# Optimization experiments

Hardware: AMD Instinct MI355X
Metric: run time of the kernel (lower is better)

## Reference

```python
import jax, jax.numpy as jnp
import numpy as np


def setup_inputs() -> dict:
    key = jax.random.key(0)
    B, T, FFT, HOP = 16, 2048, 1024, 256
    n_bins = FFT // 2 + 1  # 513
    stfts = jax.random.normal(key, (B, T, n_bins, 2), dtype=jnp.float32)
    return {"stfts": stfts, "frame_length": FFT, "frame_step": HOP, "fft_length": FFT}


def reference(stfts, frame_length, frame_step, fft_length):
    # --- precomputed constants (built in the layer's build()) ---
    n = jnp.arange(fft_length, dtype=jnp.float32)
    angles = (2.0 * np.pi / fft_length) * (n[:, None] * n[None, :])  # [fft, fft]
    idft_cos = jnp.cos(angles)
    idft_sin = jnp.sin(angles)
    # periodic Hann window
    t = jnp.arange(frame_length, dtype=jnp.float32)
    window = 0.5 - 0.5 * jnp.cos(2.0 * np.pi * t / frame_length)
    hop_ratio = frame_step / frame_length
    normalization = np.sqrt(1.0 / (1.0 - hop_ratio + 1e-8))
    syn_window = window / np.float32(normalization)
    if fft_length > frame_length:
        syn_window = jnp.pad(syn_window, (0, fft_length - frame_length))

    # --- forward ---
    real_part = stfts[..., 0]  # [B, T, n_bins]
    imag_part = stfts[..., 1]
    if fft_length % 2 == 0:
        mirror_real = real_part[:, :, 1:-1]
        mirror_imag = imag_part[:, :, 1:-1]
    else:
        mirror_real = real_part[:, :, 1:]
        mirror_imag = imag_part[:, :, 1:]
    full_real = jnp.concatenate([real_part, mirror_real[:, :, ::-1]], axis=-1)   # [B, T, fft]
    full_imag = jnp.concatenate([imag_part, -mirror_imag[:, :, ::-1]], axis=-1)  # [B, T, fft]

    # explicit IDFT via dense matmul (transpose_b in TF; matrices are symmetric)
    time_real = jnp.einsum('btf,nf->btn', full_real, idft_cos)
    time_real = time_real - jnp.einsum('btf,nf->btn', full_imag, idft_sin)
    time_real = time_real / jnp.float32(fft_length)

    windowed = (time_real * syn_window[None, None, :])[:, :, :frame_length]  # [B, T, frame_length]

    # overlap-and-add
    B, T, L = windowed.shape
    out_len = (T - 1) * frame_step + frame_length
    idx = jnp.arange(T)[:, None] * frame_step + jnp.arange(L)[None, :]  # [T, L]
    out = jnp.zeros((B, out_len), dtype=windowed.dtype).at[:, idx].add(windowed)
    return out
```

## Files before the change

kernel.cpp:

```cpp
#include <hip/hip_runtime.h>
#include <math.h>


#define BATCH  16
#define TFR    2048
#define NB     513
#define HOP    256
#define OUTLEN 525056
#define TROWS  2051
#define OWN    32
#define NBLK   65
#define OLALEN (OWN * HOP)
#define OLAPAD (OLALEN + OLALEN / 16)

#define NTHR   512
#define NWAVE  8

#define PIDX(n) ((n) + ((n) >> 4))

#define TWO_PI 6.2831853071795864f
#define WSCALE 8.456302966727588e-4f

__device__ __forceinline__ float2 cadd(float2 a, float2 b){ return make_float2(a.x+b.x, a.y+b.y); }
__device__ __forceinline__ float2 csub(float2 a, float2 b){ return make_float2(a.x-b.x, a.y-b.y); }
__device__ __forceinline__ float2 cmul(float2 a, float2 b){ return make_float2(a.x*b.x - a.y*b.y, a.x*b.y + a.y*b.x); }

__global__ __launch_bounds__(NTHR)
void istft_rfft(const float2* __restrict__ stfts, float* __restrict__ out)
{
    __shared__ float ola[OLAPAD];

    const int tid  = threadIdx.x;
    const int lane = tid & 63;
    const int wave = tid >> 6;

    const int b  = blockIdx.x / NBLK;
    const int ib = blockIdx.x - b * NBLK;
    const int T0 = ib * OWN;

    for (int i = tid; i < OLAPAD; i += NTHR) ola[i] = 0.f;

    float2 ptw[8];
    #pragma unroll
    for (int r = 0; r < 8; ++r) {
        float s, c;
        sincosf(TWO_PI * (float)(lane + 64 * r) * (1.0f / 1024.0f), &s, &c);
        ptw[r] = make_float2(c, s);
    }
    float2 om[8];
    om[0] = make_float2(1.f, 0.f);
    { float s, c; sincosf(TWO_PI * (float)lane * (1.0f / 512.0f), &s, &c); om[1] = make_float2(c, s); }
    #pragma unroll
    for (int m = 2; m < 8; ++m) om[m] = cmul(om[m - 1], om[1]);
    float2 twc[5];
    #pragma unroll
    for (int s = 0; s < 5; ++s) {
        const int h = 32 >> s;
        float sn, cs;
        sincosf(TWO_PI * (float)(lane & (h - 1)) / (float)(2 * h), &sn, &cs);
        twc[s] = (lane & h) ? make_float2(cs, sn) : make_float2(1.f, 0.f);
    }
    const int brl = ((lane & 1) << 5) | ((lane & 2) << 3) | ((lane & 4) << 1)
                  | ((lane & 8) >> 1) | ((lane & 16) >> 3) | ((lane & 32) >> 5);
    const int n0 = brl * 16;
    float win[16];
    #pragma unroll
    for (int j = 0; j < 16; ++j)
        win[j] = (0.5f - 0.5f * cosf(TWO_PI * (float)(n0 + j) * (1.0f / 1024.0f))) * WSCALE;

    __syncthreads();

    const int tmin = (T0 - 3 > 0) ? T0 - 3 : 0;
    const int tmax = (T0 + OWN - 1 < TFR - 1) ? T0 + OWN - 1 : TFR - 1;
    const int srcl = (64 - lane) & 63;

    for (int t = tmin + wave; t <= tmax; t += NWAVE) {
        const float2* Xg = stfts + (size_t)(b * TFR + t) * NB;

        float2 X[8];
        #pragma unroll
        for (int r = 0; r < 8; ++r) X[r] = Xg[lane + 64 * r];
        const float2 X512 = Xg[512];

        float2 Z[8];
        #pragma unroll
        for (int r = 0; r < 8; ++r) {
            float2 mv;
            mv.x = __shfl(X[7 - r].x, srcl);
            mv.y = __shfl(X[7 - r].y, srcl);
            const float2 fix = (r == 0) ? X512 : X[(8 - r) & 7];
            if (lane == 0) mv = fix;
            float Yy = X[r].y, Cy = -mv.y;
            if (lane == 0 && r == 0) { Yy = 0.f; Cy = 0.f; }
            const float Sx = X[r].x + mv.x, Sy = Yy + Cy;
            const float Dx = X[r].x - mv.x, Dy = Yy - Cy;
            const float2 W = ptw[r];
            const float ex = W.x * Dx - W.y * Dy;
            const float ey = W.x * Dy + W.y * Dx;
            Z[r] = make_float2(Sx - ey, Sy + ex);
        }

        float2 u[8];
        {
            const float2 t0 = cadd(Z[0], Z[4]), t1 = csub(Z[0], Z[4]);
            const float2 t2 = cadd(Z[2], Z[6]), t3 = csub(Z[2], Z[6]);
            const float2 t4 = cadd(Z[1], Z[5]), t5 = csub(Z[1], Z[5]);
            const float2 t6 = cadd(Z[3], Z[7]), t7 = csub(Z[3], Z[7]);
            const float2 E0 = cadd(t0, t2), E2 = csub(t0, t2);
            const float2 E1 = make_float2(t1.x - t3.y, t1.y + t3.x);
            const float2 E3 = make_float2(t1.x + t3.y, t1.y - t3.x);
            const float2 O0 = cadd(t4, t6), O2 = csub(t4, t6);
            const float2 O1 = make_float2(t5.x - t7.y, t5.y + t7.x);
            const float2 O3 = make_float2(t5.x + t7.y, t5.y - t7.x);
            const float cc = 0.70710678118654752f;
            const float2 W1O1 = make_float2(cc * (O1.x - O1.y), cc * (O1.x + O1.y));
            const float2 iO2  = make_float2(-O2.y, O2.x);
            const float2 W3O3 = make_float2(cc * (-O3.x - O3.y), cc * (O3.x - O3.y));
            u[0] = cadd(E0, O0);   u[4] = csub(E0, O0);
            u[1] = cadd(E1, W1O1); u[5] = csub(E1, W1O1);
            u[2] = cadd(E2, iO2);  u[6] = csub(E2, iO2);
            u[3] = cadd(E3, W3O3); u[7] = csub(E3, W3O3);
        }
        #pragma unroll
        for (int m = 1; m < 8; ++m) u[m] = cmul(u[m], om[m]);

        #pragma unroll
        for (int s = 0; s < 6; ++s) {
            const int h = 32 >> s;
            const bool lo = (lane & h) == 0;
            #pragma unroll
            for (int m = 0; m < 8; ++m) {
                const float sx = __shfl_xor(u[m].x, h);
                const float sy = __shfl_xor(u[m].y, h);
                float2 w;
                w.x = sx + (lo ? u[m].x : -u[m].x);
                w.y = sy + (lo ? u[m].y : -u[m].y);
                u[m] = (h > 1) ? cmul(w, twc[s]) : w;
            }
        }

        const int base = (t - T0) * HOP + n0;
        if ((unsigned)base < OLALEN) {
            const int pb = PIDX(base);
            #pragma unroll
            for (int m = 0; m < 8; ++m) {
                atomicAdd(&ola[pb + 2 * m],     u[m].x * win[2 * m]);
                atomicAdd(&ola[pb + 2 * m + 1], u[m].y * win[2 * m + 1]);
            }
        }
    }

    __syncthreads();

    const int ownRows = (TROWS - T0 < OWN) ? (TROWS - T0) : OWN;
    const int total   = ownRows * HOP;
    float* og = out + (size_t)b * OUTLEN + (size_t)T0 * HOP;
    for (int i = tid; i < total; i += NTHR)
        og[i] = ola[PIDX(i)];
}

extern "C" void kernel_launch(void* const* d_in, const int* in_sizes, int n_in,
                              void* d_out, int out_size, void* d_ws, size_t ws_size,
                              hipStream_t stream)
{
    const float2* stfts = reinterpret_cast<const float2*>(d_in[0]);
    float* out = reinterpret_cast<float*>(d_out);

    istft_rfft<<<dim3(BATCH * NBLK), dim3(NTHR), 0, stream>>>(stfts, out);
}
```

Before: 222.9 us.

## Derive FFT twiddles from base rotations and use DPP/permlane for butterflies

Replaces the per-thread twiddle, omega and window register arrays with a few base complex values (P, V) plus constant tables. The stage twiddles are rebuilt by repeated squaring and the window is recomputed at each atomic add. Cross-lane butterfly exchanges now use DPP row ops for distances 8, 2 and 1, and permlane32_swap (when available) for distance 32, instead of ds_bpermute shuffles. The aim is lower register pressure and cheaper lane exchanges, in exchange for extra multiplies per frame and some precision loss from the squared twiddles.

```diff
diff --git a/kernel.cpp b/kernel.cpp
--- a/kernel.cpp
+++ b/kernel.cpp
@@ -25,6 +25,44 @@
 __device__ __forceinline__ float2 csub(float2 a, float2 b){ return make_float2(a.x-b.x, a.y-b.y); }
 __device__ __forceinline__ float2 cmul(float2 a, float2 b){ return make_float2(a.x*b.x - a.y*b.y, a.x*b.y + a.y*b.x); }
 
+#if __has_builtin(__builtin_amdgcn_permlane32_swap)
+#define HAVE_PL32 1
+__device__ __forceinline__ float plsel32(float v, bool pick0) {
+    auto r = __builtin_amdgcn_permlane32_swap(
+        __builtin_bit_cast(int, v), __builtin_bit_cast(int, v), false, false);
+    return __builtin_bit_cast(float, pick0 ? r[0] : r[1]);
+}
+#else
+#define HAVE_PL32 0
+#endif
+
+template<int CTRL>
+__device__ __forceinline__ float dppf(float v) {
+    return __builtin_bit_cast(float,
+        __builtin_amdgcn_update_dpp(0, __builtin_bit_cast(int, v), CTRL, 0xF, 0xF, true));
+}
+
+__device__ __forceinline__ float2 bstep(float2 u, float2 p, bool hi, float2 W) {
+    const float2 s = cadd(u, p);
+    const float2 d = cmul(csub(u, p), W);
+    return hi ? d : s;
+}
+
+__device__ __constant__ const float W16C[8] = { 1.f, 0.9238795325112867f, 0.7071067811865476f, 0.3826834323650898f,
+                                                0.f,-0.3826834323650898f,-0.7071067811865476f,-0.9238795325112867f };
+__device__ __constant__ const float W16S[8] = { 0.f, 0.3826834323650898f, 0.7071067811865476f, 0.9238795325112867f,
+                                                1.f, 0.9238795325112867f, 0.7071067811865476f, 0.3826834323650898f };
+__device__ __constant__ const float CWT[16] = {
+    1.f, 0.9999811752826011f, 0.9999247018391445f, 0.9998305817958234f,
+    0.9996988186962042f, 0.9995294175010931f, 0.9993223845883495f, 0.9990777277526454f,
+    0.9987954562051724f, 0.9984755805732948f, 0.9981181129001492f, 0.9977230666441916f,
+    0.9972904566786902f, 0.9968202992911657f, 0.9963126121827780f, 0.9957674144676598f };
+__device__ __constant__ const float SWT[16] = {
+    0.f, 0.0061358846491545f, 0.0122715382857199f, 0.0184067299058048f,
+    0.0245412285229123f, 0.0306748031766366f, 0.0368072229413588f, 0.0429382569349408f,
+    0.0490676743274180f, 0.0551952443496899f, 0.0613207363022086f, 0.0674439195636641f,
+    0.0735645635996674f, 0.0796824379714301f, 0.0857973123444399f, 0.0919089564971327f };
+
 __global__ __launch_bounds__(NTHR)
 void istft_rfft(const float2* __restrict__ stfts, float* __restrict__ out)
 {
@@ -40,33 +78,33 @@
 
     for (int i = tid; i < OLAPAD; i += NTHR) ola[i] = 0.f;
 
-    float2 ptw[8];
-    #pragma unroll
-    for (int r = 0; r < 8; ++r) {
-        float s, c;
-        sincosf(TWO_PI * (float)(lane + 64 * r) * (1.0f / 1024.0f), &s, &c);
-        ptw[r] = make_float2(c, s);
-    }
-    float2 om[8];
-    om[0] = make_float2(1.f, 0.f);
-    { float s, c; sincosf(TWO_PI * (float)lane * (1.0f / 512.0f), &s, &c); om[1] = make_float2(c, s); }
-    #pragma unroll
-    for (int m = 2; m < 8; ++m) om[m] = cmul(om[m - 1], om[1]);
-    float2 twc[5];
-    #pragma unroll
-    for (int s = 0; s < 5; ++s) {
-        const int h = 32 >> s;
-        float sn, cs;
-        sincosf(TWO_PI * (float)(lane & (h - 1)) / (float)(2 * h), &sn, &cs);
-        twc[s] = (lane & h) ? make_float2(cs, sn) : make_float2(1.f, 0.f);
-    }
+    float2 P, V;
+    { float s, c; sincosf(TWO_PI * (float)lane * (1.0f/1024.0f), &s, &c); P = make_float2(c, s); }
     const int brl = ((lane & 1) << 5) | ((lane & 2) << 3) | ((lane & 4) << 1)
                   | ((lane & 8) >> 1) | ((lane & 16) >> 3) | ((lane & 32) >> 5);
     const int n0 = brl * 16;
-    float win[16];
-    #pragma unroll
-    for (int j = 0; j < 16; ++j)
-        win[j] = (0.5f - 0.5f * cosf(TWO_PI * (float)(n0 + j) * (1.0f / 1024.0f))) * WSCALE;
+    { float s, c; sincosf(TWO_PI * (float)n0 * (1.0f/1024.0f), &s, &c); V = make_float2(c, s); }
+
+    const float2 Q   = cmul(P, P);
+    const float2 P4  = cmul(Q, Q);
+    const float2 P8  = cmul(P4, P4);
+    const float2 B64 = cmul(P8, P8);
+    const float2 B32 = cmul(B64, B64);
+    const float2 B16 = cmul(B32, B32);
+    const float2 B8c = cmul(B16, B16);
+    const float2 B4c = cmul(B8c, B8c);
+
+#if HAVE_PL32
+    bool pick32;
+    { auto pr = __builtin_amdgcn_permlane32_swap(lane, lane, false, false);
+      pick32 = ((pr[0] == (lane & 31)) == (lane >= 32)); }
+#endif
+    const bool hi32 = lane >= 32;
+    const bool hi16 = (lane & 16) != 0;
+    const bool hi8  = (lane & 8)  != 0;
+    const bool hi4  = (lane & 4)  != 0;
+    const bool hi2  = (lane & 2)  != 0;
+    const bool hi1  = (lane & 1)  != 0;
 
     __syncthreads();
 
@@ -94,7 +132,7 @@
             if (lane == 0 && r == 0) { Yy = 0.f; Cy = 0.f; }
             const float Sx = X[r].x + mv.x, Sy = Yy + Cy;
             const float Dx = X[r].x - mv.x, Dy = Yy - Cy;
-            const float2 W = ptw[r];
+            const float2 W = cmul(P, make_float2(W16C[r], W16S[r]));
             const float ex = W.x * Dx - W.y * Dy;
             const float ey = W.x * Dy + W.y * Dx;
             Z[r] = make_float2(Sx - ey, Sy + ex);
@@ -121,22 +159,54 @@
             u[2] = cadd(E2, iO2);  u[6] = csub(E2, iO2);
             u[3] = cadd(E3, W3O3); u[7] = csub(E3, W3O3);
         }
-        #pragma unroll
-        for (int m = 1; m < 8; ++m) u[m] = cmul(u[m], om[m]);
-
-        #pragma unroll
-        for (int s = 0; s < 6; ++s) {
-            const int h = 32 >> s;
-            const bool lo = (lane & h) == 0;
-            #pragma unroll
-            for (int m = 0; m < 8; ++m) {
-                const float sx = __shfl_xor(u[m].x, h);
-                const float sy = __shfl_xor(u[m].y, h);
-                float2 w;
-                w.x = sx + (lo ? u[m].x : -u[m].x);
-                w.y = sy + (lo ? u[m].y : -u[m].y);
-                u[m] = (h > 1) ? cmul(w, twc[s]) : w;
-            }
+        {
+            const float2 om3 = cmul(P4, Q);
+            const float2 om5 = cmul(P8, Q);
+            const float2 om6 = cmul(P8, P4);
+            const float2 om7 = cmul(P8, om3);
+            u[1] = cmul(u[1], Q);
+            u[2] = cmul(u[2], P4);
+            u[3] = cmul(u[3], om3);
+            u[4] = cmul(u[4], P8);
+            u[5] = cmul(u[5], om5);
+            u[6] = cmul(u[6], om6);
+            u[7] = cmul(u[7], om7);
+        }
+
+        #pragma unroll
+        for (int m = 0; m < 8; ++m) {
+            float2 p;
+#if HAVE_PL32
+            p = make_float2(plsel32(u[m].x, pick32), plsel32(u[m].y, pick32));
+#else
+            p = make_float2(__shfl_xor(u[m].x, 32), __shfl_xor(u[m].y, 32));
+#endif
+            u[m] = bstep(u[m], p, hi32, B64);
+        }
+        #pragma unroll
+        for (int m = 0; m < 8; ++m) {
+            const float2 p = make_float2(__shfl_xor(u[m].x, 16), __shfl_xor(u[m].y, 16));
+            u[m] = bstep(u[m], p, hi16, B32);
+        }
+        #pragma unroll
+        for (int m = 0; m < 8; ++m) {
+            const float2 p = make_float2(dppf<0x128>(u[m].x), dppf<0x128>(u[m].y));
+            u[m] = bstep(u[m], p, hi8, B16);
+        }
+        #pragma unroll
+        for (int m = 0; m < 8; ++m) {
+            const float2 p = make_float2(__shfl_xor(u[m].x, 4), __shfl_xor(u[m].y, 4));
+            u[m] = bstep(u[m], p, hi4, B8c);
+        }
+        #pragma unroll
+        for (int m = 0; m < 8; ++m) {
+            const float2 p = make_float2(dppf<0x4E>(u[m].x), dppf<0x4E>(u[m].y));
+            u[m] = bstep(u[m], p, hi2, B4c);
+        }
+        #pragma unroll
+        for (int m = 0; m < 8; ++m) {
+            const float2 p = make_float2(dppf<0xB1>(u[m].x), dppf<0xB1>(u[m].y));
+            u[m] = hi1 ? csub(p, u[m]) : cadd(u[m], p);
         }
 
         const int base = (t - T0) * HOP + n0;
@@ -144,8 +214,10 @@
             const int pb = PIDX(base);
             #pragma unroll
             for (int m = 0; m < 8; ++m) {
-                atomicAdd(&ola[pb + 2 * m],     u[m].x * win[2 * m]);
-                atomicAdd(&ola[pb + 2 * m + 1], u[m].y * win[2 * m + 1]);
+                const float w0 = 0.5f * WSCALE * (1.f - (V.x * CWT[2*m]   - V.y * SWT[2*m]));
+                const float w1 = 0.5f * WSCALE * (1.f - (V.x * CWT[2*m+1] - V.y * SWT[2*m+1]));
+                atomicAdd(&ola[pb + 2*m],     u[m].x * w0);
+                atomicAdd(&ola[pb + 2*m + 1], u[m].y * w1);
             }
         }
     }
```

Measured after the change: 206.0 us. 1.08x faster.
